# Performance work log

Hardware: AMD Instinct MI355X
Metric: run time of the kernel (lower is better)

Reference implementation:

```python
import jax, jax.numpy as jnp
import numpy as np

HID = 64
EPS = 1e-12  # tf.contrib.layers.layer_norm variance_epsilon


def _ln(x, g, b):
    m = jnp.mean(x, axis=-1, keepdims=True)
    v = jnp.mean(jnp.square(x - m), axis=-1, keepdims=True)
    return (x - m) * jax.lax.rsqrt(v + EPS) * g + b


def setup_inputs() -> dict:
    key = jax.random.key(0)
    k1, k2, k3, k4 = jax.random.split(key, 4)
    N, T, OBS, ACT = 2048, 256, 96, 32
    D = OBS + ACT
    obss = jax.random.normal(k1, (N, T, OBS), dtype=jnp.float32)
    actions = jax.random.normal(k2, (N, T, ACT), dtype=jnp.float32)
    W = jax.random.normal(k3, (D + HID, 4 * HID), dtype=jnp.float32) * (1.0 / np.sqrt(D + HID))
    ln_gamma = jnp.ones((5, HID), dtype=jnp.float32)   # i, j, f, o, state norms
    ln_beta = jnp.zeros((5, HID), dtype=jnp.float32)
    dense_W = jax.random.uniform(k4, (HID, 1), dtype=jnp.float32, minval=-0.003, maxval=0.003)
    dense_b = jnp.zeros((1,), dtype=jnp.float32)
    return {"obss": obss, "actions": actions, "W": W, "ln_gamma": ln_gamma,
            "ln_beta": ln_beta, "dense_W": dense_W, "dense_b": dense_b}


def reference(obss, actions, W, ln_gamma, ln_beta, dense_W, dense_b):
    # [N,T,obs+act] -> time-major [T,N,D]
    x = jnp.concatenate([obss, actions], axis=-1)
    xt = jnp.transpose(x, (1, 0, 2))
    N = x.shape[0]
    c0 = jnp.zeros((N, HID), dtype=x.dtype)
    h0 = jnp.zeros((N, HID), dtype=x.dtype)
    forget_bias = jnp.asarray(1.0, dtype=x.dtype)

    def step(carry, x_t):
        c, h = carry
        z = jnp.concatenate([x_t, h], axis=-1) @ W  # [N, 4*HID], no bias
        i, j, f, o = jnp.split(z, 4, axis=-1)
        i = _ln(i, ln_gamma[0], ln_beta[0])
        j = _ln(j, ln_gamma[1], ln_beta[1])
        f = _ln(f, ln_gamma[2], ln_beta[2])
        o = _ln(o, ln_gamma[3], ln_beta[3])
        new_c = c * jax.nn.sigmoid(f + forget_bias) + jax.nn.sigmoid(i) * jnp.tanh(j)
        new_c = _ln(new_c, ln_gamma[4], ln_beta[4])
        new_h = jnp.tanh(new_c) * jax.nn.sigmoid(o)
        return (new_c, new_h), new_h

    _, hs = jax.lax.scan(step, (c0, h0), xt)  # hs: [T,N,HID]
    outputs = jnp.transpose(hs, (1, 0, 2))     # [N,T,HID]
    q = outputs @ dense_W + dense_b            # [N,T,1]
    return q
```

## Files before the change

kernel.cpp:

```cpp
#include <hip/hip_runtime.h>

#define TT 256
#define OBS 96
#define ACTD 32
#define HID 64
#define XHP 200
#define EPS 1e-12f

typedef __bf16 bf16x8 __attribute__((ext_vector_type(8)));
typedef float f32x4 __attribute__((ext_vector_type(4)));
typedef unsigned short u16x8 __attribute__((ext_vector_type(8)));
typedef unsigned int u32;
typedef unsigned short u16;

__device__ __forceinline__ u16 f2bf(float f) {
  u32 x = __builtin_bit_cast(u32, f);
  x += 0x7fffu + ((x >> 16) & 1u);
  return (u16)(x >> 16);
}
__device__ __forceinline__ u32 pk2bf(float a, float b) {
  return (u32)f2bf(a) | ((u32)f2bf(b) << 16);
}
__device__ __forceinline__ float sigm(float x) { return 1.0f / (1.0f + __expf(-x)); }
__device__ __forceinline__ float tanh_(float x) { return 1.0f - 2.0f / (__expf(2.0f * x) + 1.0f); }

__global__ __launch_bounds__(256, 1) void lstm_fused(
    const float* __restrict__ obss, const float* __restrict__ actions,
    const float* __restrict__ Wm, const float* __restrict__ gamma,
    const float* __restrict__ beta, const float* __restrict__ dWv,
    const float* __restrict__ dbv, float* __restrict__ out)
{
  __shared__ u16 xh[16 * XHP];
  __shared__ float gates[4][8][64];
  __shared__ float cst[8][64];

  const int tid = threadIdx.x;
  const int wv = tid >> 6;
  const int ln = tid & 63;
  const int l15 = ln & 15;
  const int quad = ln >> 4;
  const int n0 = blockIdx.x * 8;

  for (int i = tid; i < 16 * XHP / 2; i += 256) ((u32*)xh)[i] = 0u;
  for (int i = tid; i < 8 * 64; i += 256) ((float*)cst)[i] = 0.0f;

  u16x8 bw[6][4];
  #pragma unroll
  for (int kt = 0; kt < 6; ++kt) {
    #pragma unroll
    for (int nt = 0; nt < 4; ++nt) {
      #pragma unroll
      for (int j = 0; j < 8; ++j) {
        float v = Wm[(kt * 32 + quad * 8 + j) * 256 + wv * 64 + nt * 16 + l15];
        bw[kt][nt][j] = f2bf(v);
      }
    }
  }

  float gg[4], gb[4];
  #pragma unroll
  for (int nt = 0; nt < 4; ++nt) {
    gg[nt] = gamma[wv * 64 + nt * 16 + l15];
    gb[nt] = beta[wv * 64 + nt * 16 + l15];
  }

  const int em = tid >> 5;
  const int ec = (tid & 31) * 2;
  const float cg0 = gamma[4 * 64 + ec], cg1 = gamma[4 * 64 + ec + 1];
  const float cb0 = beta[4 * 64 + ec],  cb1 = beta[4 * 64 + ec + 1];
  const float dw0 = dWv[ec], dw1 = dWv[ec + 1];
  const float bias = dbv[0];

  const int xr = tid >> 5;
  const int xq = tid & 31;
  const float* obs_p = obss + (size_t)(n0 + xr) * TT * OBS;
  const float* act_p = actions + (size_t)(n0 + xr) * TT * ACTD;

  __syncthreads();

  {
    f32x4 x0;
    if (xq < 24) x0 = *(const f32x4*)(obs_p + xq * 4);
    else         x0 = *(const f32x4*)(act_p + (xq - 24) * 4);
    u32* dst = (u32*)(xh + xr * XHP + xq * 4);
    dst[0] = pk2bf(x0[0], x0[1]);
    dst[1] = pk2bf(x0[2], x0[3]);
  }
  __syncthreads();

  for (int t = 0; t < TT; ++t) {
    const int tn = (t < TT - 1) ? t + 1 : t;
    f32x4 xnx;
    if (xq < 24) xnx = *(const f32x4*)(obs_p + tn * OBS + xq * 4);
    else         xnx = *(const f32x4*)(act_p + tn * ACTD + (xq - 24) * 4);

    u16x8 af[6];
    #pragma unroll
    for (int kt = 0; kt < 6; ++kt)
      af[kt] = *(const u16x8*)(xh + l15 * XHP + kt * 32 + quad * 8);

    f32x4 acc[4];
    #pragma unroll
    for (int nt = 0; nt < 4; ++nt) {
      f32x4 a = {0.0f, 0.0f, 0.0f, 0.0f};
      #pragma unroll
      for (int kt = 0; kt < 6; ++kt)
        a = __builtin_amdgcn_mfma_f32_16x16x32_bf16(
            __builtin_bit_cast(bf16x8, af[kt]),
            __builtin_bit_cast(bf16x8, bw[kt][nt]), a, 0, 0, 0);
      acc[nt] = a;
    }

    float s[4], ss[4];
    #pragma unroll
    for (int r = 0; r < 4; ++r) {
      s[r]  = acc[0][r] + acc[1][r] + acc[2][r] + acc[3][r];
      ss[r] = acc[0][r] * acc[0][r] + acc[1][r] * acc[1][r] +
              acc[2][r] * acc[2][r] + acc[3][r] * acc[3][r];
    }
    #pragma unroll
    for (int msk = 1; msk <= 8; msk <<= 1) {
      #pragma unroll
      for (int r = 0; r < 4; ++r) {
        s[r]  += __shfl_xor(s[r],  msk);
        ss[r] += __shfl_xor(ss[r], msk);
      }
    }
    if (ln < 32) {
      #pragma unroll
      for (int r = 0; r < 4; ++r) {
        const float mean = s[r] * (1.0f / 64.0f);
        const float var  = ss[r] * (1.0f / 64.0f) - mean * mean;
        const float rstd = rsqrtf(var + EPS);
        const int row = quad * 4 + r;
        #pragma unroll
        for (int nt = 0; nt < 4; ++nt)
          gates[wv][row][nt * 16 + l15] = (acc[nt][r] - mean) * rstd * gg[nt] + gb[nt];
      }
    }
    __syncthreads();

    const float2 iv = *(const float2*)&gates[0][em][ec];
    const float2 jv = *(const float2*)&gates[1][em][ec];
    const float2 fv = *(const float2*)&gates[2][em][ec];
    const float2 ov = *(const float2*)&gates[3][em][ec];
    const float2 cv = *(const float2*)&cst[em][ec];
    float nc0 = cv.x * sigm(fv.x + 1.0f) + sigm(iv.x) * tanh_(jv.x);
    float nc1 = cv.y * sigm(fv.y + 1.0f) + sigm(iv.y) * tanh_(jv.y);
    float s2 = nc0 + nc1, ss2 = nc0 * nc0 + nc1 * nc1;
    #pragma unroll
    for (int msk = 1; msk <= 16; msk <<= 1) {
      s2  += __shfl_xor(s2,  msk);
      ss2 += __shfl_xor(ss2, msk);
    }
    const float mean = s2 * (1.0f / 64.0f);
    const float var  = ss2 * (1.0f / 64.0f) - mean * mean;
    const float rstd = rsqrtf(var + EPS);
    const float c0 = (nc0 - mean) * rstd * cg0 + cb0;
    const float c1 = (nc1 - mean) * rstd * cg1 + cb1;
    *(float2*)&cst[em][ec] = make_float2(c0, c1);
    const float h0 = tanh_(c0) * sigm(ov.x);
    const float h1 = tanh_(c1) * sigm(ov.y);
    *(u32*)(xh + em * XHP + 128 + ec) = pk2bf(h0, h1);

    float qp = h0 * dw0 + h1 * dw1;
    #pragma unroll
    for (int msk = 1; msk <= 16; msk <<= 1)
      qp += __shfl_xor(qp, msk);
    if ((tid & 31) == 0) out[(size_t)(n0 + em) * TT + t] = qp + bias;

    {
      u32* dst = (u32*)(xh + xr * XHP + xq * 4);
      dst[0] = pk2bf(xnx[0], xnx[1]);
      dst[1] = pk2bf(xnx[2], xnx[3]);
    }
    __syncthreads();
  }
}

extern "C" void kernel_launch(void* const* d_in, const int* in_sizes, int n_in,
                              void* d_out, int out_size, void* d_ws, size_t ws_size,
                              hipStream_t stream) {
  const float* obss    = (const float*)d_in[0];
  const float* actions = (const float*)d_in[1];
  const float* Wm      = (const float*)d_in[2];
  const float* gamma   = (const float*)d_in[3];
  const float* beta    = (const float*)d_in[4];
  const float* dWv     = (const float*)d_in[5];
  const float* dbv     = (const float*)d_in[6];
  float* out = (float*)d_out;
  lstm_fused<<<dim3(256), dim3(256), 0, stream>>>(obss, actions, Wm, gamma, beta,
                                                  dWv, dbv, out);
}
```

Before: 725.0 us.

## Halve rows per block to 4, use DPP reductions, and split cell/load waves

Drops the batch rows per block from 8 to 4, so the grid doubles to 512 blocks and launch bounds allow two blocks per CU. This spreads the latency-bound recurrence across more CUs and waves. Row-sum reductions now use DPP row operations in place of shuffle chains. The cell update runs on the first two waves while the other two stage the next timestep's inputs, so those steps overlap. The cost is that MFMA tiles are only a quarter filled (4 of 16 rows), and the per-wave weight registers must now fit a two-blocks-per-CU budget.

```diff
diff --git a/kernel.cpp b/kernel.cpp
--- a/kernel.cpp
+++ b/kernel.cpp
@@ -4,6 +4,7 @@
 #define OBS 96
 #define ACTD 32
 #define HID 64
+#define RPB 4
 #define XHP 200
 #define EPS 1e-12f
 
@@ -24,38 +25,52 @@
 __device__ __forceinline__ float sigm(float x) { return 1.0f / (1.0f + __expf(-x)); }
 __device__ __forceinline__ float tanh_(float x) { return 1.0f - 2.0f / (__expf(2.0f * x) + 1.0f); }
 
-__global__ __launch_bounds__(256, 1) void lstm_fused(
+template <int CTRL>
+__device__ __forceinline__ float dpp_add(float x) {
+  int t = __builtin_amdgcn_update_dpp(0, __builtin_bit_cast(int, x), CTRL, 0xF, 0xF, true);
+  return x + __builtin_bit_cast(float, t);
+}
+__device__ __forceinline__ float red16(float x) {
+  x = dpp_add<0xB1>(x);
+  x = dpp_add<0x4E>(x);
+  x = dpp_add<0x124>(x);
+  x = dpp_add<0x128>(x);
+  return x;
+}
+__device__ __forceinline__ float red32(float x) {
+  x = red16(x);
+  x += __shfl_xor(x, 16, 64);
+  return x;
+}
+
+__global__ __launch_bounds__(256, 2) void lstm_fused(
     const float* __restrict__ obss, const float* __restrict__ actions,
     const float* __restrict__ Wm, const float* __restrict__ gamma,
     const float* __restrict__ beta, const float* __restrict__ dWv,
     const float* __restrict__ dbv, float* __restrict__ out)
 {
   __shared__ u16 xh[16 * XHP];
-  __shared__ float gates[4][8][64];
-  __shared__ float cst[8][64];
+  __shared__ float gates[4][RPB][64];
+  __shared__ float cst[RPB][64];
 
   const int tid = threadIdx.x;
   const int wv = tid >> 6;
   const int ln = tid & 63;
   const int l15 = ln & 15;
   const int quad = ln >> 4;
-  const int n0 = blockIdx.x * 8;
+  const int n0 = blockIdx.x * RPB;
 
   for (int i = tid; i < 16 * XHP / 2; i += 256) ((u32*)xh)[i] = 0u;
-  for (int i = tid; i < 8 * 64; i += 256) ((float*)cst)[i] = 0.0f;
+  for (int i = tid; i < RPB * 64; i += 256) ((float*)cst)[i] = 0.0f;
 
   u16x8 bw[6][4];
   #pragma unroll
-  for (int kt = 0; kt < 6; ++kt) {
+  for (int kt = 0; kt < 6; ++kt)
     #pragma unroll
-    for (int nt = 0; nt < 4; ++nt) {
+    for (int nt = 0; nt < 4; ++nt)
       #pragma unroll
-      for (int j = 0; j < 8; ++j) {
-        float v = Wm[(kt * 32 + quad * 8 + j) * 256 + wv * 64 + nt * 16 + l15];
-        bw[kt][nt][j] = f2bf(v);
-      }
-    }
-  }
+      for (int j = 0; j < 8; ++j)
+        bw[kt][nt][j] = f2bf(Wm[(kt * 32 + quad * 8 + j) * 256 + wv * 64 + nt * 16 + l15]);
 
   float gg[4], gb[4];
   #pragma unroll
@@ -64,21 +79,22 @@
     gb[nt] = beta[wv * 64 + nt * 16 + l15];
   }
 
-  const int em = tid >> 5;
+  const int crow = tid >> 5;
   const int ec = (tid & 31) * 2;
   const float cg0 = gamma[4 * 64 + ec], cg1 = gamma[4 * 64 + ec + 1];
   const float cb0 = beta[4 * 64 + ec],  cb1 = beta[4 * 64 + ec + 1];
   const float dw0 = dWv[ec], dw1 = dWv[ec + 1];
   const float bias = dbv[0];
 
-  const int xr = tid >> 5;
-  const int xq = tid & 31;
+  const int lt = tid & 127;
+  const int xr = lt >> 5;
+  const int xq = lt & 31;
   const float* obs_p = obss + (size_t)(n0 + xr) * TT * OBS;
   const float* act_p = actions + (size_t)(n0 + xr) * TT * ACTD;
 
   __syncthreads();
 
-  {
+  if (tid >= 128) {
     f32x4 x0;
     if (xq < 24) x0 = *(const f32x4*)(obs_p + xq * 4);
     else         x0 = *(const f32x4*)(act_p + (xq - 24) * 4);
@@ -91,8 +107,10 @@
   for (int t = 0; t < TT; ++t) {
     const int tn = (t < TT - 1) ? t + 1 : t;
     f32x4 xnx;
-    if (xq < 24) xnx = *(const f32x4*)(obs_p + tn * OBS + xq * 4);
-    else         xnx = *(const f32x4*)(act_p + tn * ACTD + (xq - 24) * 4);
+    if (tid >= 128) {
+      if (xq < 24) xnx = *(const f32x4*)(obs_p + tn * OBS + xq * 4);
+      else         xnx = *(const f32x4*)(act_p + tn * ACTD + (xq - 24) * 4);
+    }
 
     u16x8 af[6];
     #pragma unroll
@@ -117,59 +135,45 @@
       s[r]  = acc[0][r] + acc[1][r] + acc[2][r] + acc[3][r];
       ss[r] = acc[0][r] * acc[0][r] + acc[1][r] * acc[1][r] +
               acc[2][r] * acc[2][r] + acc[3][r] * acc[3][r];
+      s[r]  = red16(s[r]);
+      ss[r] = red16(ss[r]);
     }
-    #pragma unroll
-    for (int msk = 1; msk <= 8; msk <<= 1) {
+    if (ln < 16) {
       #pragma unroll
-      for (int r = 0; r < 4; ++r) {
-        s[r]  += __shfl_xor(s[r],  msk);
-        ss[r] += __shfl_xor(ss[r], msk);
-      }
-    }
-    if (ln < 32) {
-      #pragma unroll
-      for (int r = 0; r < 4; ++r) {
+      for (int r = 0; r < RPB; ++r) {
         const float mean = s[r] * (1.0f / 64.0f);
         const float var  = ss[r] * (1.0f / 64.0f) - mean * mean;
         const float rstd = rsqrtf(var + EPS);
-        const int row = quad * 4 + r;
         #pragma unroll
         for (int nt = 0; nt < 4; ++nt)
-          gates[wv][row][nt * 16 + l15] = (acc[nt][r] - mean) * rstd * gg[nt] + gb[nt];
+          gates[wv][r][nt * 16 + l15] = (acc[nt][r] - mean) * rstd * gg[nt] + gb[nt];
       }
     }
     __syncthreads();
 
-    const float2 iv = *(const float2*)&gates[0][em][ec];
-    const float2 jv = *(const float2*)&gates[1][em][ec];
-    const float2 fv = *(const float2*)&gates[2][em][ec];
-    const float2 ov = *(const float2*)&gates[3][em][ec];
-    const float2 cv = *(const float2*)&cst[em][ec];
-    float nc0 = cv.x * sigm(fv.x + 1.0f) + sigm(iv.x) * tanh_(jv.x);
-    float nc1 = cv.y * sigm(fv.y + 1.0f) + sigm(iv.y) * tanh_(jv.y);
-    float s2 = nc0 + nc1, ss2 = nc0 * nc0 + nc1 * nc1;
-    #pragma unroll
-    for (int msk = 1; msk <= 16; msk <<= 1) {
-      s2  += __shfl_xor(s2,  msk);
-      ss2 += __shfl_xor(ss2, msk);
-    }
-    const float mean = s2 * (1.0f / 64.0f);
-    const float var  = ss2 * (1.0f / 64.0f) - mean * mean;
-    const float rstd = rsqrtf(var + EPS);
-    const float c0 = (nc0 - mean) * rstd * cg0 + cb0;
-    const float c1 = (nc1 - mean) * rstd * cg1 + cb1;
-    *(float2*)&cst[em][ec] = make_float2(c0, c1);
-    const float h0 = tanh_(c0) * sigm(ov.x);
-    const float h1 = tanh_(c1) * sigm(ov.y);
-    *(u32*)(xh + em * XHP + 128 + ec) = pk2bf(h0, h1);
+    if (tid < 128) {
+      const float2 iv = *(const float2*)&gates[0][crow][ec];
+      const float2 jv = *(const float2*)&gates[1][crow][ec];
+      const float2 fv = *(const float2*)&gates[2][crow][ec];
+      const float2 ov = *(const float2*)&gates[3][crow][ec];
+      const float2 cv = *(const float2*)&cst[crow][ec];
+      const float nc0 = cv.x * sigm(fv.x + 1.0f) + sigm(iv.x) * tanh_(jv.x);
+      const float nc1 = cv.y * sigm(fv.y + 1.0f) + sigm(iv.y) * tanh_(jv.y);
+      float s2  = red32(nc0 + nc1);
+      float ss2 = red32(nc0 * nc0 + nc1 * nc1);
+      const float mean = s2 * (1.0f / 64.0f);
+      const float var  = ss2 * (1.0f / 64.0f) - mean * mean;
+      const float rstd = rsqrtf(var + EPS);
+      const float c0 = (nc0 - mean) * rstd * cg0 + cb0;
+      const float c1 = (nc1 - mean) * rstd * cg1 + cb1;
+      *(float2*)&cst[crow][ec] = make_float2(c0, c1);
+      const float h0 = tanh_(c0) * sigm(ov.x);
+      const float h1 = tanh_(c1) * sigm(ov.y);
+      *(u32*)(xh + crow * XHP + 128 + ec) = pk2bf(h0, h1);
 
-    float qp = h0 * dw0 + h1 * dw1;
-    #pragma unroll
-    for (int msk = 1; msk <= 16; msk <<= 1)
-      qp += __shfl_xor(qp, msk);
-    if ((tid & 31) == 0) out[(size_t)(n0 + em) * TT + t] = qp + bias;
-
-    {
+      float qp = red32(h0 * dw0 + h1 * dw1);
+      if ((tid & 31) == 0) out[(size_t)(n0 + crow) * TT + t] = qp + bias;
+    } else {
       u32* dst = (u32*)(xh + xr * XHP + xq * 4);
       dst[0] = pk2bf(xnx[0], xnx[1]);
       dst[1] = pk2bf(xnx[2], xnx[3]);
@@ -189,6 +193,6 @@
   const float* dWv     = (const float*)d_in[5];
   const float* dbv     = (const float*)d_in[6];
   float* out = (float*)d_out;
-  lstm_fused<<<dim3(256), dim3(256), 0, stream>>>(obss, actions, Wm, gamma, beta,
-                                                  dWv, dbv, out);
+  lstm_fused<<<dim3(2048 / RPB), dim3(256), 0, stream>>>(obss, actions, Wm, gamma,
+                                                         beta, dWv, dbv, out);
 }
```

Result: slower. 750.5 us (+3.5%).
